# Kernel tuning notes

Measured on AMD Instinct MI355X. Metric: run time of the kernel, lower is better.

Reference implementation:

```python
import jax, jax.numpy as jnp
import numpy as np
import math

B, S, D, H = 2, 2048, 1024, 16
DK = D // H
EPS = 1e-6
TEMPERATURE = 1.0


def layernorm(x, a2, b2):
    # torch LayerNorm-variant: unbiased std (ddof=1), eps added to std
    mean = jnp.mean(x, axis=-1, keepdims=True)
    std = jnp.std(x, axis=-1, keepdims=True, ddof=1)
    return a2 * (x - mean) / (std + EPS) + b2


def setup_inputs() -> dict:
    key = jax.random.key(0)
    ks = jax.random.split(key, 12)
    scale = 1.0 / math.sqrt(D)
    inp = {
        "k": jax.random.normal(ks[0], (B, S, D), jnp.float32),
        "q": jax.random.normal(ks[1], (B, S, D), jnp.float32),
        "v": jax.random.normal(ks[2], (B, S, D), jnp.float32),
        "mask": jax.random.randint(ks[3], (B, S, S), 0, 2, jnp.int32),
        "Wq": jax.random.normal(ks[4], (D, D), jnp.float32) * scale,
        "bq": jnp.zeros((D,), jnp.float32),
        "Wk": jax.random.normal(ks[5], (D, D), jnp.float32) * scale,
        "bk": jnp.zeros((D,), jnp.float32),
        "Wv": jax.random.normal(ks[6], (D, D), jnp.float32) * scale,
        "bv": jnp.zeros((D,), jnp.float32),
        "Wo": jax.random.normal(ks[7], (D, D), jnp.float32) * scale,
        "bo": jnp.zeros((D,), jnp.float32),
        "a2": jnp.ones((D,), jnp.float32),
        "b2": jnp.zeros((D,), jnp.float32),
    }
    return inp


def reference(k, q, v, mask, Wq, bq, Wk, bk, Wv, bv, Wo, bo, a2, b2):
    # pre-norm all three streams
    kn = layernorm(k, a2, b2)
    qn = layernorm(q, a2, b2)
    vn = layernorm(v, a2, b2)
    # NOTE original quirk: linears[0](k)->query, linears[1](q)->key, linears[2](v)->value
    def proj(x, W, b):  # [B,S,D] -> [B,H,S,DK]
        y = x @ W + b
        return y.reshape(B, S, H, DK).transpose(0, 2, 1, 3)
    query = proj(kn, Wq, bq)
    key_ = proj(qn, Wk, bk)
    value = proj(vn, Wv, bv)
    scores = jnp.einsum('bhqd,bhkd->bhqk', query, key_) / math.sqrt(DK)
    scores = jnp.where(mask[:, None, :, :] == 0, jnp.float32(-1e9), scores)
    p_attn = jax.nn.softmax(scores * TEMPERATURE, axis=-1)
    x = jnp.einsum('bhqk,bhkd->bhqd', p_attn, value)
    x = x.transpose(0, 2, 1, 3).reshape(B, S, D)
    return x @ Wo + bo + vn  # residual adds normalized v
```

## Files before the change

kernel.cpp:

```cpp
#include <hip/hip_runtime.h>
#include <hip/hip_bf16.h>

#define B_  2
#define S_  2048
#define D_  1024
#define H_  16
#define DK_ 64
#define M_  4096

using bf16x8 = __attribute__((ext_vector_type(8))) __bf16;
using f32x4  = __attribute__((ext_vector_type(4))) float;

typedef __attribute__((address_space(1))) void gvoid;
typedef __attribute__((address_space(3))) void lvoid;

__device__ __forceinline__ void gload_lds16(const void* g, void* l) {
  __builtin_amdgcn_global_load_lds((gvoid*)g, (lvoid*)l, 16, 0, 0);
}

__device__ __forceinline__ f32x4 mfma16(bf16x8 a, bf16x8 b, f32x4 c) {
  return __builtin_amdgcn_mfma_f32_16x16x32_bf16(a, b, c, 0, 0, 0);
}

__device__ __forceinline__ int swz64(int row, int ce) {
  return row * 64 + ((((ce >> 3) ^ (row & 7)) << 3) | (ce & 7));
}

__global__ __launch_bounds__(256) void ln3_kernel(
    const float* __restrict__ kin, const float* __restrict__ qin,
    const float* __restrict__ vin,
    const float* __restrict__ a2, const float* __restrict__ b2,
    __hip_bfloat16* __restrict__ kn, __hip_bfloat16* __restrict__ qn,
    __hip_bfloat16* __restrict__ vnb, float* __restrict__ vnf)
{
  const int row = blockIdx.x;
  const int st  = blockIdx.y;
  const float* src = (st == 0) ? kin : (st == 1) ? qin : vin;
  const int t = threadIdx.x;
  const size_t base = (size_t)row * D_;

  float4 x = *(const float4*)(src + base + t * 4);
  float s  = x.x + x.y + x.z + x.w;
  float s2 = x.x * x.x + x.y * x.y + x.z * x.z + x.w * x.w;
  #pragma unroll
  for (int off = 32; off >= 1; off >>= 1) {
    s  += __shfl_down(s,  off, 64);
    s2 += __shfl_down(s2, off, 64);
  }
  __shared__ float red[4][2];
  __shared__ float stats[2];
  const int wid = t >> 6, lane = t & 63;
  if (lane == 0) { red[wid][0] = s; red[wid][1] = s2; }
  __syncthreads();
  if (t == 0) {
    float S  = red[0][0] + red[1][0] + red[2][0] + red[3][0];
    float S2 = red[0][1] + red[1][1] + red[2][1] + red[3][1];
    float mean = S * (1.0f / D_);
    float var  = fmaxf((S2 - S * mean) * (1.0f / (D_ - 1)), 0.0f);
    stats[0] = mean;
    stats[1] = 1.0f / (sqrtf(var) + 1e-6f);
  }
  __syncthreads();
  const float mean = stats[0], inv = stats[1];
  float4 ga = *(const float4*)(a2 + t * 4);
  float4 gb = *(const float4*)(b2 + t * 4);
  float o0 = ga.x * (x.x - mean) * inv + gb.x;
  float o1 = ga.y * (x.y - mean) * inv + gb.y;
  float o2 = ga.z * (x.z - mean) * inv + gb.z;
  float o3 = ga.w * (x.w - mean) * inv + gb.w;
  __hip_bfloat16* dst = (st == 0) ? kn : (st == 1) ? qn : vnb;
  union { __hip_bfloat16 h[4]; ushort4 u; } pk;
  pk.h[0] = __float2bfloat16(o0); pk.h[1] = __float2bfloat16(o1);
  pk.h[2] = __float2bfloat16(o2); pk.h[3] = __float2bfloat16(o3);
  *reinterpret_cast<ushort4*>((unsigned short*)dst + base + t * 4) = pk.u;
  if (st == 2) {
    float4 of = make_float4(o0, o1, o2, o3);
    *reinterpret_cast<float4*>(vnf + base + t * 4) = of;
  }
}

__global__ __launch_bounds__(256) void pack_mask_kernel(
    const int* __restrict__ mask, unsigned int* __restrict__ bits)
{
  const int w = blockIdx.x * 256 + threadIdx.x;
  const int* src = mask + (size_t)w * 32;
  unsigned int acc = 0;
  #pragma unroll
  for (int j = 0; j < 32; j += 4) {
    int4 t = *(const int4*)(src + j);
    acc |= (t.x != 0 ? 1u : 0u) << (j + 0);
    acc |= (t.y != 0 ? 1u : 0u) << (j + 1);
    acc |= (t.z != 0 ? 1u : 0u) << (j + 2);
    acc |= (t.w != 0 ? 1u : 0u) << (j + 3);
  }
  bits[w] = acc;
}

__global__ __launch_bounds__(256) void wt_cast_kernel(
    const float* __restrict__ W0, const float* __restrict__ W1,
    const float* __restrict__ W2, const float* __restrict__ W3,
    __hip_bfloat16* __restrict__ T0, __hip_bfloat16* __restrict__ T1,
    __hip_bfloat16* __restrict__ T2, __hip_bfloat16* __restrict__ T3)
{
  const int z = blockIdx.z;
  const float* W = (z == 0) ? W0 : (z == 1) ? W1 : (z == 2) ? W2 : W3;
  __hip_bfloat16* T = (z == 0) ? T0 : (z == 1) ? T1 : (z == 2) ? T2 : T3;
  __shared__ float tile[32][33];
  const int k0 = blockIdx.y * 32, n0 = blockIdx.x * 32;
  const int tx = threadIdx.x & 31, ty = threadIdx.x >> 5;
  #pragma unroll
  for (int i = ty; i < 32; i += 8)
    tile[i][tx] = W[(size_t)(k0 + i) * D_ + n0 + tx];
  __syncthreads();
  #pragma unroll
  for (int i = ty; i < 32; i += 8)
    T[(size_t)(n0 + i) * D_ + k0 + tx] = __float2bfloat16(tile[tx][i]);
}

__global__ __launch_bounds__(256) void proj3_kernel(
    const __hip_bfloat16* __restrict__ kn, const __hip_bfloat16* __restrict__ qn,
    const __hip_bfloat16* __restrict__ vnb,
    const __hip_bfloat16* __restrict__ Wqt, const __hip_bfloat16* __restrict__ Wkt,
    const __hip_bfloat16* __restrict__ Wvt,
    const float* __restrict__ bq, const float* __restrict__ bk,
    const float* __restrict__ bv,
    __hip_bfloat16* __restrict__ Qb, __hip_bfloat16* __restrict__ Kb,
    __hip_bfloat16* __restrict__ Vtb)
{
  const int z = blockIdx.z;
  const __hip_bfloat16* A  = (z == 0) ? kn  : (z == 1) ? qn  : vnb;
  const __hip_bfloat16* Wt = (z == 0) ? Wqt : (z == 1) ? Wkt : Wvt;
  const float* bias = (z == 0) ? bq : (z == 1) ? bk : bv;
  const float scale = (z == 0) ? 0.125f : 1.0f;

  __shared__ __hip_bfloat16 As[128 * 32];
  __shared__ __hip_bfloat16 Bs[128 * 32];
  const int n0 = blockIdx.x * 128;
  const int m0 = blockIdx.y * 128;
  const int tid = threadIdx.x;
  const int wid = tid >> 6, lane = tid & 63;
  const int wm = wid >> 1, wn = wid & 1;
  const int srow = lane >> 2;
  const int scol = (lane & 3) * 8;
  const int fr = lane & 15, fk8 = (lane >> 4) * 8, fq = lane >> 4;

  f32x4 acc[4][4] = {};

  for (int kt = 0; kt < D_ / 32; ++kt) {
    const int k0 = kt * 32;
    #pragma unroll
    for (int p = 0; p < 2; ++p) {
      const int r0 = 32 * wid + 16 * p;
      gload_lds16(A  + (size_t)(m0 + r0 + srow) * D_ + k0 + scol, &As[r0 * 32]);
      gload_lds16(Wt + (size_t)(n0 + r0 + srow) * D_ + k0 + scol, &Bs[r0 * 32]);
    }
    __syncthreads();
    bf16x8 af[4], bfr[4];
    #pragma unroll
    for (int i = 0; i < 4; ++i)
      af[i] = *(const bf16x8*)&As[(64 * wm + 16 * i + fr) * 32 + fk8];
    #pragma unroll
    for (int j = 0; j < 4; ++j)
      bfr[j] = *(const bf16x8*)&Bs[(64 * wn + 16 * j + fr) * 32 + fk8];
    #pragma unroll
    for (int i = 0; i < 4; ++i)
      #pragma unroll
      for (int j = 0; j < 4; ++j)
        acc[i][j] = mfma16(af[i], bfr[j], acc[i][j]);
    __syncthreads();
  }

  #pragma unroll
  for (int i = 0; i < 4; ++i) {
    #pragma unroll
    for (int j = 0; j < 4; ++j) {
      const int n = n0 + 64 * wn + 16 * j + fr;
      const float bn = bias[n];
      const int h = n >> 6, d = n & (DK_ - 1);
      #pragma unroll
      for (int r = 0; r < 4; ++r) {
        const int m = m0 + 64 * wm + 16 * i + 4 * fq + r;
        const int b = m >> 11, sl = m & (S_ - 1);
        const float val = (acc[i][j][r] + bn) * scale;
        if (z < 2) {
          __hip_bfloat16* dst = (z == 0) ? Qb : Kb;
          dst[((size_t)(b * H_ + h) * S_ + sl) * DK_ + d] = __float2bfloat16(val);
        } else {
          Vtb[((size_t)(b * H_ + h) * DK_ + d) * S_ + sl] = __float2bfloat16(val);
        }
      }
    }
  }
}

__global__ __launch_bounds__(256) void gemm_out_kernel(
    const __hip_bfloat16* __restrict__ A,
    const __hip_bfloat16* __restrict__ Wt,
    const float* __restrict__ bias,
    const float* __restrict__ residf,
    float* __restrict__ dst)
{
  __shared__ __hip_bfloat16 As[128 * 32];
  __shared__ __hip_bfloat16 Bs[128 * 32];
  const int n0 = blockIdx.x * 128;
  const int m0 = blockIdx.y * 128;
  const int tid = threadIdx.x;
  const int wid = tid >> 6, lane = tid & 63;
  const int wm = wid >> 1, wn = wid & 1;
  const int srow = lane >> 2;
  const int scol = (lane & 3) * 8;
  const int fr = lane & 15, fk8 = (lane >> 4) * 8, fq = lane >> 4;

  f32x4 acc[4][4] = {};

  for (int kt = 0; kt < D_ / 32; ++kt) {
    const int k0 = kt * 32;
    #pragma unroll
    for (int p = 0; p < 2; ++p) {
      const int r0 = 32 * wid + 16 * p;
      gload_lds16(A  + (size_t)(m0 + r0 + srow) * D_ + k0 + scol, &As[r0 * 32]);
      gload_lds16(Wt + (size_t)(n0 + r0 + srow) * D_ + k0 + scol, &Bs[r0 * 32]);
    }
    __syncthreads();
    bf16x8 af[4], bfr[4];
    #pragma unroll
    for (int i = 0; i < 4; ++i)
      af[i] = *(const bf16x8*)&As[(64 * wm + 16 * i + fr) * 32 + fk8];
    #pragma unroll
    for (int j = 0; j < 4; ++j)
      bfr[j] = *(const bf16x8*)&Bs[(64 * wn + 16 * j + fr) * 32 + fk8];
    #pragma unroll
    for (int i = 0; i < 4; ++i)
      #pragma unroll
      for (int j = 0; j < 4; ++j)
        acc[i][j] = mfma16(af[i], bfr[j], acc[i][j]);
    __syncthreads();
  }

  #pragma unroll
  for (int i = 0; i < 4; ++i) {
    #pragma unroll
    for (int j = 0; j < 4; ++j) {
      const int n = n0 + 64 * wn + 16 * j + fr;
      const float bn = bias[n];
      #pragma unroll
      for (int r = 0; r < 4; ++r) {
        const int m = m0 + 64 * wm + 16 * i + 4 * fq + r;
        dst[(size_t)m * D_ + n] =
            acc[i][j][r] + bn + residf[(size_t)m * D_ + n];
      }
    }
  }
}

__global__ __launch_bounds__(256) void attn_kernel(
    const __hip_bfloat16* __restrict__ Qb,
    const __hip_bfloat16* __restrict__ Kb,
    const __hip_bfloat16* __restrict__ Vtb,
    const unsigned int* __restrict__ mbits,
    __hip_bfloat16* __restrict__ Ob)
{
  __shared__ __hip_bfloat16 Qs[64 * 64];
  __shared__ __hip_bfloat16 Ks[64 * 64];
  __shared__ __hip_bfloat16 Vs[64 * 64];
  __shared__ __hip_bfloat16 Ps[4][16 * 64];

  const int q0 = blockIdx.x * 64;
  const int bh = blockIdx.y;
  const int b = bh >> 4;
  const int h = bh & 15;
  const int tid = threadIdx.x, wid = tid >> 6, lane = tid & 63;
  const __hip_bfloat16* qp = Qb  + (size_t)bh * S_ * DK_;
  const __hip_bfloat16* kp = Kb  + (size_t)bh * S_ * DK_;
  const __hip_bfloat16* vp = Vtb + (size_t)bh * DK_ * S_;

  const int srow = lane >> 3;
  const int scol = ((lane & 7) ^ (lane >> 3)) << 3;
  const int fr = lane & 15, fq = lane >> 4, fk8 = fq * 8;

  const unsigned int* mrow = mbits + (size_t)b * S_ * (S_ / 32)
                           + (size_t)(q0 + 16 * wid + 4 * fq) * (S_ / 32);

  #pragma unroll
  for (int p = 0; p < 2; ++p) {
    const int r0 = 16 * wid + 8 * p;
    gload_lds16(qp + (size_t)(q0 + r0 + srow) * DK_ + scol, &Qs[r0 * 64]);
  }

  float lrun[4] = {0.0f, 0.0f, 0.0f, 0.0f};
  f32x4 acc[4] = {};

  __syncthreads();

  for (int kt = 0; kt < S_ / 64; ++kt) {
    const int k0 = kt * 64;
    #pragma unroll
    for (int p = 0; p < 2; ++p) {
      const int r0 = 16 * wid + 8 * p;
      gload_lds16(kp + (size_t)(k0 + r0 + srow) * DK_ + scol, &Ks[r0 * 64]);
      gload_lds16(vp + (size_t)(r0 + srow) * S_ + k0 + scol,  &Vs[r0 * 64]);
    }
    __syncthreads();

    f32x4 sf[4] = {};
    __builtin_amdgcn_s_setprio(1);
    #pragma unroll
    for (int ks = 0; ks < 2; ++ks) {
      const bf16x8 aq = *(const bf16x8*)&Qs[swz64(16 * wid + fr, ks * 32 + fk8)];
      #pragma unroll
      for (int ni = 0; ni < 4; ++ni) {
        const bf16x8 bk = *(const bf16x8*)&Ks[swz64(16 * ni + fr, ks * 32 + fk8)];
        sf[ni] = mfma16(aq, bk, sf[ni]);
      }
    }
    __builtin_amdgcn_s_setprio(0);

    unsigned int wm0[4], wm1[4];
    #pragma unroll
    for (int r = 0; r < 4; ++r) {
      wm0[r] = mrow[(size_t)r * (S_ / 32) + 2 * kt];
      wm1[r] = mrow[(size_t)r * (S_ / 32) + 2 * kt + 1];
    }
    #pragma unroll
    for (int ni = 0; ni < 4; ++ni) {
      const int c = 16 * ni + fr;
      #pragma unroll
      for (int r = 0; r < 4; ++r) {
        float p = __expf(sf[ni][r]);
        const unsigned int bit = (((c < 32) ? wm0[r] : wm1[r]) >> (c & 31)) & 1u;
        p = bit ? p : 0.0f;
        lrun[r] += p;
        Ps[wid][swz64(4 * fq + r, c)] = __float2bfloat16(p);
      }
    }

    __builtin_amdgcn_s_setprio(1);
    #pragma unroll
    for (int ks = 0; ks < 2; ++ks) {
      const bf16x8 ap = *(const bf16x8*)&Ps[wid][swz64(fr, ks * 32 + fk8)];
      #pragma unroll
      for (int di = 0; di < 4; ++di) {
        const bf16x8 bv = *(const bf16x8*)&Vs[swz64(16 * di + fr, ks * 32 + fk8)];
        acc[di] = mfma16(ap, bv, acc[di]);
      }
    }
    __builtin_amdgcn_s_setprio(0);
    __syncthreads();
  }

  #pragma unroll
  for (int off = 1; off < 16; off <<= 1)
    #pragma unroll
    for (int r = 0; r < 4; ++r)
      lrun[r] += __shfl_xor(lrun[r], off, 64);

  #pragma unroll
  for (int di = 0; di < 4; ++di)
    #pragma unroll
    for (int r = 0; r < 4; ++r) {
      const int qg = q0 + 16 * wid + 4 * fq + r;
      Ob[((size_t)b * S_ + qg) * D_ + h * DK_ + 16 * di + fr] =
          __float2bfloat16(acc[di][r] / lrun[r]);
    }
}

extern "C" void kernel_launch(void* const* d_in, const int* in_sizes, int n_in,
                              void* d_out, int out_size, void* d_ws, size_t ws_size,
                              hipStream_t stream)
{
  const float* k    = (const float*)d_in[0];
  const float* q    = (const float*)d_in[1];
  const float* v    = (const float*)d_in[2];
  const int*   mask = (const int*)  d_in[3];
  const float* Wq   = (const float*)d_in[4];
  const float* bq   = (const float*)d_in[5];
  const float* Wk   = (const float*)d_in[6];
  const float* bk   = (const float*)d_in[7];
  const float* Wv   = (const float*)d_in[8];
  const float* bv   = (const float*)d_in[9];
  const float* Wo   = (const float*)d_in[10];
  const float* bo   = (const float*)d_in[11];
  const float* a2   = (const float*)d_in[12];
  const float* b2   = (const float*)d_in[13];

  char* ws = (char*)d_ws;
  const size_t MB = (size_t)1 << 20;
  __hip_bfloat16* kn   = (__hip_bfloat16*)(ws + 0 * MB);
  __hip_bfloat16* qn   = (__hip_bfloat16*)(ws + 8 * MB);
  __hip_bfloat16* vnb  = (__hip_bfloat16*)(ws + 16 * MB);
  __hip_bfloat16* Wqt  = (__hip_bfloat16*)(ws + 24 * MB);
  __hip_bfloat16* Wkt  = (__hip_bfloat16*)(ws + 26 * MB);
  __hip_bfloat16* Wvt  = (__hip_bfloat16*)(ws + 28 * MB);
  __hip_bfloat16* Wot  = (__hip_bfloat16*)(ws + 30 * MB);
  __hip_bfloat16* Qb   = (__hip_bfloat16*)(ws + 32 * MB);
  __hip_bfloat16* Kb   = (__hip_bfloat16*)(ws + 40 * MB);
  __hip_bfloat16* Vtb  = (__hip_bfloat16*)(ws + 48 * MB);
  __hip_bfloat16* Ob   = (__hip_bfloat16*)(ws + 56 * MB);
  unsigned int*   mbts = (unsigned int*)  (ws + 64 * MB);
  float*          vnf  = (float*)         (ws + 66 * MB);

  ln3_kernel<<<dim3(M_, 3), 256, 0, stream>>>(k, q, v, a2, b2, kn, qn, vnb, vnf);
  pack_mask_kernel<<<dim3(B_ * S_ * (S_ / 32) / 256), 256, 0, stream>>>(mask, mbts);
  wt_cast_kernel<<<dim3(32, 32, 4), 256, 0, stream>>>(Wq, Wk, Wv, Wo, Wqt, Wkt, Wvt, Wot);

  proj3_kernel<<<dim3(8, 32, 3), 256, 0, stream>>>(
      kn, qn, vnb, Wqt, Wkt, Wvt, bq, bk, bv, Qb, Kb, Vtb);

  attn_kernel<<<dim3(S_ / 64, B_ * H_), 256, 0, stream>>>(Qb, Kb, Vtb, mbts, Ob);

  gemm_out_kernel<<<dim3(8, 32), 256, 0, stream>>>(Ob, Wot, bo, vnf, (float*)d_out);
}
```

Before: 301.5 us.

## Load attention K/V fragments directly from global into registers, drop LDS staging

The attention kernel no longer stages Q, K and V tiles through shared memory with block-wide barriers. Each wave now reads its MFMA operand fragments straight from global memory (through the caches) into registers, which removes the per-tile __syncthreads. Separately, log2(e) is folded into the query projection scale so the softmax can use exp2f instead of __expf. Every wave now loads the same K/V data redundantly from global memory, relying on L1/L2 hits, and the loads are no longer overlapped with compute the way the async LDS copies were.

```diff
diff --git a/kernel.cpp b/kernel.cpp
--- a/kernel.cpp
+++ b/kernel.cpp
@@ -131,7 +131,7 @@
   const __hip_bfloat16* A  = (z == 0) ? kn  : (z == 1) ? qn  : vnb;
   const __hip_bfloat16* Wt = (z == 0) ? Wqt : (z == 1) ? Wkt : Wvt;
   const float* bias = (z == 0) ? bq : (z == 1) ? bk : bv;
-  const float scale = (z == 0) ? 0.125f : 1.0f;
+  const float scale = (z == 0) ? 0.125f * 1.44269504088896340736f : 1.0f;
 
   __shared__ __hip_bfloat16 As[128 * 32];
   __shared__ __hip_bfloat16 Bs[128 * 32];
@@ -260,9 +260,6 @@
     const unsigned int* __restrict__ mbits,
     __hip_bfloat16* __restrict__ Ob)
 {
-  __shared__ __hip_bfloat16 Qs[64 * 64];
-  __shared__ __hip_bfloat16 Ks[64 * 64];
-  __shared__ __hip_bfloat16 Vs[64 * 64];
   __shared__ __hip_bfloat16 Ps[4][16 * 64];
 
   const int q0 = blockIdx.x * 64;
@@ -274,46 +271,47 @@
   const __hip_bfloat16* kp = Kb  + (size_t)bh * S_ * DK_;
   const __hip_bfloat16* vp = Vtb + (size_t)bh * DK_ * S_;
 
-  const int srow = lane >> 3;
-  const int scol = ((lane & 7) ^ (lane >> 3)) << 3;
   const int fr = lane & 15, fq = lane >> 4, fk8 = fq * 8;
 
   const unsigned int* mrow = mbits + (size_t)b * S_ * (S_ / 32)
                            + (size_t)(q0 + 16 * wid + 4 * fq) * (S_ / 32);
 
-  #pragma unroll
-  for (int p = 0; p < 2; ++p) {
-    const int r0 = 16 * wid + 8 * p;
-    gload_lds16(qp + (size_t)(q0 + r0 + srow) * DK_ + scol, &Qs[r0 * 64]);
-  }
+  bf16x8 aq[2];
+  #pragma unroll
+  for (int ks = 0; ks < 2; ++ks)
+    aq[ks] = *(const bf16x8*)(qp + (size_t)(q0 + 16 * wid + fr) * DK_
+                                 + ks * 32 + fk8);
 
   float lrun[4] = {0.0f, 0.0f, 0.0f, 0.0f};
   f32x4 acc[4] = {};
 
-  __syncthreads();
-
   for (int kt = 0; kt < S_ / 64; ++kt) {
     const int k0 = kt * 64;
-    #pragma unroll
-    for (int p = 0; p < 2; ++p) {
-      const int r0 = 16 * wid + 8 * p;
-      gload_lds16(kp + (size_t)(k0 + r0 + srow) * DK_ + scol, &Ks[r0 * 64]);
-      gload_lds16(vp + (size_t)(r0 + srow) * S_ + k0 + scol,  &Vs[r0 * 64]);
-    }
-    __syncthreads();
+
+    bf16x8 kf[2][4];
+    #pragma unroll
+    for (int ks = 0; ks < 2; ++ks)
+      #pragma unroll
+      for (int ni = 0; ni < 4; ++ni)
+        kf[ks][ni] = *(const bf16x8*)(kp + (size_t)(k0 + 16 * ni + fr) * DK_
+                                         + ks * 32 + fk8);
 
     f32x4 sf[4] = {};
     __builtin_amdgcn_s_setprio(1);
     #pragma unroll
-    for (int ks = 0; ks < 2; ++ks) {
-      const bf16x8 aq = *(const bf16x8*)&Qs[swz64(16 * wid + fr, ks * 32 + fk8)];
-      #pragma unroll
-      for (int ni = 0; ni < 4; ++ni) {
-        const bf16x8 bk = *(const bf16x8*)&Ks[swz64(16 * ni + fr, ks * 32 + fk8)];
-        sf[ni] = mfma16(aq, bk, sf[ni]);
-      }
-    }
+    for (int ks = 0; ks < 2; ++ks)
+      #pragma unroll
+      for (int ni = 0; ni < 4; ++ni)
+        sf[ni] = mfma16(aq[ks], kf[ks][ni], sf[ni]);
     __builtin_amdgcn_s_setprio(0);
+
+    bf16x8 vf[2][4];
+    #pragma unroll
+    for (int ks = 0; ks < 2; ++ks)
+      #pragma unroll
+      for (int di = 0; di < 4; ++di)
+        vf[ks][di] = *(const bf16x8*)(vp + (size_t)(16 * di + fr) * S_
+                                         + k0 + ks * 32 + fk8);
 
     unsigned int wm0[4], wm1[4];
     #pragma unroll
@@ -326,7 +324,7 @@
       const int c = 16 * ni + fr;
       #pragma unroll
       for (int r = 0; r < 4; ++r) {
-        float p = __expf(sf[ni][r]);
+        float p = exp2f(sf[ni][r]);
         const unsigned int bit = (((c < 32) ? wm0[r] : wm1[r]) >> (c & 31)) & 1u;
         p = bit ? p : 0.0f;
         lrun[r] += p;
@@ -339,13 +337,10 @@
     for (int ks = 0; ks < 2; ++ks) {
       const bf16x8 ap = *(const bf16x8*)&Ps[wid][swz64(fr, ks * 32 + fk8)];
       #pragma unroll
-      for (int di = 0; di < 4; ++di) {
-        const bf16x8 bv = *(const bf16x8*)&Vs[swz64(16 * di + fr, ks * 32 + fk8)];
-        acc[di] = mfma16(ap, bv, acc[di]);
-      }
+      for (int di = 0; di < 4; ++di)
+        acc[di] = mfma16(ap, vf[ks][di], acc[di]);
     }
     __builtin_amdgcn_s_setprio(0);
-    __syncthreads();
   }
 
   #pragma unroll
```

Result: slower. 481.7 us (+59.8%).

## Double-buffer K/V tiles in attention, keep Q in registers, use exp2

Applied to the files above, without the earlier changes.

The attention kernel now prefetches the next K/V tile into a second LDS buffer while the current tile is processed. This removes the load-then-barrier stall at the start of each iteration. Q fragments are loaded once into registers instead of staged through LDS. The log2(e) factor is folded into the Q projection scale so softmax can use exp2f. The cost is doubled K/V LDS usage, which may reduce occupancy.

```diff
diff --git a/kernel.cpp b/kernel.cpp
--- a/kernel.cpp
+++ b/kernel.cpp
@@ -131,7 +131,7 @@
   const __hip_bfloat16* A  = (z == 0) ? kn  : (z == 1) ? qn  : vnb;
   const __hip_bfloat16* Wt = (z == 0) ? Wqt : (z == 1) ? Wkt : Wvt;
   const float* bias = (z == 0) ? bq : (z == 1) ? bk : bv;
-  const float scale = (z == 0) ? 0.125f : 1.0f;
+  const float scale = (z == 0) ? 0.125f * 1.44269504088896340736f : 1.0f;
 
   __shared__ __hip_bfloat16 As[128 * 32];
   __shared__ __hip_bfloat16 Bs[128 * 32];
@@ -260,9 +260,8 @@
     const unsigned int* __restrict__ mbits,
     __hip_bfloat16* __restrict__ Ob)
 {
-  __shared__ __hip_bfloat16 Qs[64 * 64];
-  __shared__ __hip_bfloat16 Ks[64 * 64];
-  __shared__ __hip_bfloat16 Vs[64 * 64];
+  __shared__ __hip_bfloat16 Ks[2][64 * 64];
+  __shared__ __hip_bfloat16 Vs[2][64 * 64];
   __shared__ __hip_bfloat16 Ps[4][16 * 64];
 
   const int q0 = blockIdx.x * 64;
@@ -281,36 +280,41 @@
   const unsigned int* mrow = mbits + (size_t)b * S_ * (S_ / 32)
                            + (size_t)(q0 + 16 * wid + 4 * fq) * (S_ / 32);
 
-  #pragma unroll
-  for (int p = 0; p < 2; ++p) {
-    const int r0 = 16 * wid + 8 * p;
-    gload_lds16(qp + (size_t)(q0 + r0 + srow) * DK_ + scol, &Qs[r0 * 64]);
-  }
+  bf16x8 aq[2];
+  #pragma unroll
+  for (int ks = 0; ks < 2; ++ks)
+    aq[ks] = *(const bf16x8*)(qp + (size_t)(q0 + 16 * wid + fr) * DK_
+                                 + ks * 32 + fk8);
+
+  auto stage = [&](int kt, int buf) {
+    const int k0 = kt * 64;
+    #pragma unroll
+    for (int p = 0; p < 2; ++p) {
+      const int r0 = 16 * wid + 8 * p;
+      gload_lds16(kp + (size_t)(k0 + r0 + srow) * DK_ + scol, &Ks[buf][r0 * 64]);
+      gload_lds16(vp + (size_t)(r0 + srow) * S_ + k0 + scol,  &Vs[buf][r0 * 64]);
+    }
+  };
 
   float lrun[4] = {0.0f, 0.0f, 0.0f, 0.0f};
   f32x4 acc[4] = {};
 
+  stage(0, 0);
   __syncthreads();
 
+  int cur = 0;
   for (int kt = 0; kt < S_ / 64; ++kt) {
-    const int k0 = kt * 64;
-    #pragma unroll
-    for (int p = 0; p < 2; ++p) {
-      const int r0 = 16 * wid + 8 * p;
-      gload_lds16(kp + (size_t)(k0 + r0 + srow) * DK_ + scol, &Ks[r0 * 64]);
-      gload_lds16(vp + (size_t)(r0 + srow) * S_ + k0 + scol,  &Vs[r0 * 64]);
-    }
-    __syncthreads();
+    if (kt + 1 < S_ / 64) stage(kt + 1, cur ^ 1);
 
     f32x4 sf[4] = {};
     __builtin_amdgcn_s_setprio(1);
     #pragma unroll
     for (int ks = 0; ks < 2; ++ks) {
-      const bf16x8 aq = *(const bf16x8*)&Qs[swz64(16 * wid + fr, ks * 32 + fk8)];
       #pragma unroll
       for (int ni = 0; ni < 4; ++ni) {
-        const bf16x8 bk = *(const bf16x8*)&Ks[swz64(16 * ni + fr, ks * 32 + fk8)];
-        sf[ni] = mfma16(aq, bk, sf[ni]);
+        const bf16x8 bk =
+            *(const bf16x8*)&Ks[cur][swz64(16 * ni + fr, ks * 32 + fk8)];
+        sf[ni] = mfma16(aq[ks], bk, sf[ni]);
       }
     }
     __builtin_amdgcn_s_setprio(0);
@@ -326,7 +330,7 @@
       const int c = 16 * ni + fr;
       #pragma unroll
       for (int r = 0; r < 4; ++r) {
-        float p = __expf(sf[ni][r]);
+        float p = exp2f(sf[ni][r]);
         const unsigned int bit = (((c < 32) ? wm0[r] : wm1[r]) >> (c & 31)) & 1u;
         p = bit ? p : 0.0f;
         lrun[r] += p;
@@ -340,12 +344,15 @@
       const bf16x8 ap = *(const bf16x8*)&Ps[wid][swz64(fr, ks * 32 + fk8)];
       #pragma unroll
       for (int di = 0; di < 4; ++di) {
-        const bf16x8 bv = *(const bf16x8*)&Vs[swz64(16 * di + fr, ks * 32 + fk8)];
+        const bf16x8 bv =
+            *(const bf16x8*)&Vs[cur][swz64(16 * di + fr, ks * 32 + fk8)];
         acc[di] = mfma16(ap, bv, acc[di]);
       }
     }
     __builtin_amdgcn_s_setprio(0);
+
     __syncthreads();
+    cur ^= 1;
   }
 
   #pragma unroll
```

After: 325.5 us. 8.0% more time.
